# Optimization experiments

Measured on AMD Instinct MI355X. Metric: run time of the kernel, lower is better.

The kernel has to match this reference:

```python
import jax, jax.numpy as jnp
import numpy as np

D = 128          # node feature dim (input_dim)
ATT_NUM = 2      # number of attention heads (att_num)
ATT_TIMES = 2    # attention refinement iterations (att_times)
K = 1            # interact_dim from att_style 'ntn_1'
DIN2 = D * ATT_NUM   # NTN input dim = 256
FMAP = 16        # feature_map_dim
B = 8            # number of graph pairs
N = 100000       # nodes per graph
EPS = 1e-12      # F.normalize eps


def _glorot(key, shape):
    fan_in, fan_out = shape[-1], shape[-2] if len(shape) > 1 else shape[-1]
    std = np.sqrt(2.0 / (fan_in + fan_out)).astype(np.float32)
    return jax.random.normal(key, shape, dtype=jnp.float32) * std


def setup_inputs() -> dict:
    key = jax.random.key(0)
    ks = jax.random.split(key, 16)
    inp = {
        "x1": jax.random.normal(ks[0], (B, N, D), dtype=jnp.float32),
        "x2": jax.random.normal(ks[1], (B, N, D), dtype=jnp.float32),
        # Attention params (stacked over att_num heads)
        "W_att": _glorot(ks[2], (ATT_NUM, D, D)),
        "V_att": _glorot(ks[3], (ATT_NUM, K, 2 * D)),
        "Wt_att": _glorot(ks[4], (ATT_NUM, K, D, D)),
        "U_att": _glorot(ks[5], (ATT_NUM, K, 1)),
        "b_att": jax.random.normal(ks[6], (ATT_NUM, K), dtype=jnp.float32) * 0.1,
        # NTN params
        "V_ntn": _glorot(ks[7], (FMAP, 2 * DIN2)),
        "W_ntn": _glorot(ks[8], (FMAP, DIN2, DIN2)),
        "b_ntn": jax.random.normal(ks[9], (FMAP,), dtype=jnp.float32),
        # projection MLP: 16 -> 8 -> 4 -> 2 -> 1 (Linear, no bias; weight shape (out, in))
        "proj0": _glorot(ks[10], (8, 16)),
        "proj1": _glorot(ks[11], (4, 8)),
        "proj2": _glorot(ks[12], (2, 4)),
        "proj3": _glorot(ks[13], (1, 2)),
    }
    return inp


def _l1_normalize(s, axis):
    return s / jnp.maximum(jnp.sum(jnp.abs(s), axis=axis, keepdims=True), EPS)


def _attention(x, W_att, V_att, Wt_att, U_att, b_att):
    # x: (N, D)  ->  pooled graph embedding (D * ATT_NUM,)
    outs = []
    for i in range(ATT_NUM):
        xc = x
        out = None
        Va, Vb = V_att[i, :, :D], V_att[i, :, D:]   # (K, D) each
        for _ in range(ATT_TIMES):
            h = jnp.tanh(jnp.mean(xc, axis=0) @ W_att[i])        # (D,)
            # NTN-style attention scores, vectorized over all nodes
            s = xc @ Va.T + (Vb @ h)[None, :]                    # (N, K)
            s = s + jnp.einsum('nd,kde,e->nk', xc, Wt_att[i], h)
            s = s + b_att[i][None, :]
            s = _l1_normalize(s, axis=1)
            att = jax.nn.sigmoid(s) @ U_att[i]                   # (N, 1)
            out = att[:, 0] @ xc                                 # (D,)
            xc = xc * att
        outs.append(out)
    return jnp.concatenate(outs)   # (DIN2,)


def _ntn(g1, g2, V_ntn, W_ntn, b_ntn):
    # g1, g2: (DIN2,) -> (FMAP,)
    Va, Vb = V_ntn[:, :DIN2], V_ntn[:, DIN2:]
    s = Va @ g1 + Vb @ g2 + jnp.einsum('fde,d,e->f', W_ntn, g1, g2) + b_ntn
    s = s / jnp.maximum(jnp.sum(jnp.abs(s)), EPS)   # L1 normalize over the single row
    return jax.nn.relu(s)


def reference(x1, x2, W_att, V_att, Wt_att, U_att, b_att,
              V_ntn, W_ntn, b_ntn, proj0, proj1, proj2, proj3):
    def pair_fn(xa, xb):
        g1 = _attention(xa, W_att, V_att, Wt_att, U_att, b_att)
        g2 = _attention(xb, W_att, V_att, Wt_att, U_att, b_att)
        y = _ntn(g1, g2, V_ntn, W_ntn, b_ntn)      # (FMAP,)
        for Wp in (proj0, proj1, proj2, proj3):
            y = Wp @ y
        return y                                    # (1,)
    return jax.vmap(pair_fn)(x1, x2)                # (B, 1) pairwise similarity scores
```

## Files before the change

kernel.cpp:

```cpp
#include <hip/hip_runtime.h>
#include <hip/hip_bf16.h>
#include <math.h>

#define NROWS 100000
#define DIM 128
#define NGRAPH 16
#define NCHUNK 128
#define CHROWS 782
#define EPSV 1e-12f

#define SZ_SUMP (NGRAPH*NCHUNK*DIM)
#define SZ_WV   (NGRAPH*2*DIM)
#define SZ_OP   (NGRAPH*NCHUNK*2*DIM)
#define OFF_SUMP 0
#define OFF_WV1 (OFF_SUMP + SZ_SUMP)
#define OFF_C1  (OFF_WV1 + SZ_WV)
#define OFF_O1P (OFF_C1 + 32)
#define OFF_WV2 (OFF_O1P + SZ_OP)
#define OFF_C2  (OFF_WV2 + SZ_WV)
#define OFF_O2P (OFF_C2 + 32)
#define OFF_G   (OFF_O2P + SZ_OP)
#define OFF_S   (OFF_G + NGRAPH*256)

__device__ __forceinline__ const float* graph_ptr(const float* x1, const float* x2, int g) {
    return (g < 8) ? (x1 + (size_t)g * NROWS * DIM) : (x2 + (size_t)(g - 8) * NROWS * DIM);
}

__device__ __forceinline__ float red16(float x) {
    int t;
    t = __builtin_amdgcn_update_dpp(0, __float_as_int(x), 0xB1, 0xF, 0xF, true);
    x += __int_as_float(t);
    t = __builtin_amdgcn_update_dpp(0, __float_as_int(x), 0x4E, 0xF, 0xF, true);
    x += __int_as_float(t);
    t = __builtin_amdgcn_update_dpp(0, __float_as_int(x), 0x141, 0xF, 0xF, true);
    x += __int_as_float(t);
    t = __builtin_amdgcn_update_dpp(0, __float_as_int(x), 0x140, 0xF, 0xF, true);
    x += __int_as_float(t);
    return x;
}

__device__ __forceinline__ float dot8(float4 v0, float4 v1, float4 w0, float4 w1) {
    float d = v0.x * w0.x;
    d = fmaf(v0.y, w0.y, d); d = fmaf(v0.z, w0.z, d); d = fmaf(v0.w, w0.w, d);
    d = fmaf(v1.x, w1.x, d); d = fmaf(v1.y, w1.y, d); d = fmaf(v1.z, w1.z, d);
    d = fmaf(v1.w, w1.w, d);
    return d;
}

__device__ __forceinline__ float4 ld4(const float* p) {
    return *reinterpret_cast<const float4*>(p);
}

__global__ __launch_bounds__(256) void k_sum(const float* __restrict__ x1,
                                             const float* __restrict__ x2,
                                             float* __restrict__ sump) {
    int g = blockIdx.x >> 7, c = blockIdx.x & (NCHUNK - 1);
    const float* xg = graph_ptr(x1, x2, g);
    int lane = threadIdx.x & 31, grp = threadIdx.x >> 5;
    int col = lane * 4;
    float ax = 0.f, ay = 0.f, az = 0.f, aw = 0.f;
    int r0 = c * CHROWS, r1 = min(r0 + CHROWS, NROWS);
    for (int r = r0 + grp; r < r1; r += 8) {
        float4 v = ld4(xg + (size_t)r * DIM + col);
        ax += v.x; ay += v.y; az += v.z; aw += v.w;
    }
    __shared__ float4 lds[256];
    lds[threadIdx.x] = make_float4(ax, ay, az, aw);
    __syncthreads();
    if (threadIdx.x < 32) {
        float4 t = lds[threadIdx.x];
        for (int k = 1; k < 8; ++k) {
            float4 o = lds[k * 32 + threadIdx.x];
            t.x += o.x; t.y += o.y; t.z += o.z; t.w += o.w;
        }
        *reinterpret_cast<float4*>(sump + ((size_t)g * NCHUNK + c) * DIM + threadIdx.x * 4) = t;
    }
}

__global__ __launch_bounds__(128) void k_prep(const float* __restrict__ src, int phase,
                                              const float* __restrict__ W_att,
                                              const float* __restrict__ V_att,
                                              const float* __restrict__ Wt_att,
                                              const float* __restrict__ b_att,
                                              float* __restrict__ wv, float* __restrict__ cc) {
    int g = blockIdx.x >> 1, i = blockIdx.x & 1;
    int t = threadIdx.x;
    __shared__ float mean[DIM], h[DIM], red[DIM];
    float s = 0.f;
    if (phase == 1) {
        for (int c = 0; c < NCHUNK; ++c) s += src[((size_t)g * NCHUNK + c) * DIM + t];
    } else {
        for (int c = 0; c < NCHUNK; ++c) s += src[(((size_t)g * NCHUNK + c) * 2 + i) * DIM + t];
    }
    mean[t] = s / (float)NROWS;
    __syncthreads();
    const float* W = W_att + (size_t)i * DIM * DIM;
    float hv = 0.f;
    for (int d = 0; d < DIM; ++d) hv = fmaf(mean[d], W[d * DIM + t], hv);
    h[t] = tanhf(hv);
    __syncthreads();
    const float* Va = V_att + (size_t)i * 2 * DIM;
    const float* Vb = Va + DIM;
    const float* Wt = Wt_att + (size_t)i * DIM * DIM;
    float w = Va[t];
    for (int e = 0; e < DIM; ++e) w = fmaf(Wt[t * DIM + e], h[e], w);
    wv[((size_t)g * 2 + i) * DIM + t] = w;
    red[t] = Vb[t] * h[t];
    __syncthreads();
    for (int k = 64; k; k >>= 1) { if (t < k) red[t] += red[t + k]; __syncthreads(); }
    if (t == 0) cc[g * 2 + i] = red[0] + b_att[i];
}

__global__ __launch_bounds__(256) void k_pass2(const float* __restrict__ x1,
                                               const float* __restrict__ x2,
                                               const float* __restrict__ wv1,
                                               const float* __restrict__ c1,
                                               const float* __restrict__ U_att,
                                               float* __restrict__ o1p) {
    int g = blockIdx.x >> 7, c = blockIdx.x & (NCHUNK - 1);
    const float* xg = graph_ptr(x1, x2, g);
    int tid = threadIdx.x;
    int l16 = tid & 15, slot = tid >> 4;
    int colb = l16 * 8;
    float4 w0a = ld4(wv1 + ((size_t)g * 2 + 0) * DIM + colb);
    float4 w0b = ld4(wv1 + ((size_t)g * 2 + 0) * DIM + colb + 4);
    float4 w1a = ld4(wv1 + ((size_t)g * 2 + 1) * DIM + colb);
    float4 w1b = ld4(wv1 + ((size_t)g * 2 + 1) * DIM + colb + 4);
    float cc0 = c1[g * 2 + 0], cc1 = c1[g * 2 + 1];
    float u0 = U_att[0], u1 = U_att[1];
    float sp = 1.f / (1.f + expf(-1.f)), sn = 1.f / (1.f + expf(1.f));
    float ap0 = u0 * sp, an0 = u0 * sn, ap1 = u1 * sp, an1 = u1 * sn;
    float4 a0l = make_float4(0, 0, 0, 0), a0h = make_float4(0, 0, 0, 0);
    float4 a1l = make_float4(0, 0, 0, 0), a1h = make_float4(0, 0, 0, 0);
    int r0 = c * CHROWS, r1 = min(r0 + CHROWS, NROWS);
    for (int r = r0 + slot; r < r1; r += 16) {
        const float* p = xg + (size_t)r * DIM + colb;
        float4 v0 = ld4(p), v1 = ld4(p + 4);
        float d0 = red16(dot8(v0, v1, w0a, w0b));
        float d1 = red16(dot8(v0, v1, w1a, w1b));
        float at0 = (d0 + cc0 >= 0.f) ? ap0 : an0;
        float at1 = (d1 + cc1 >= 0.f) ? ap1 : an1;
        a0l.x = fmaf(at0, v0.x, a0l.x); a0l.y = fmaf(at0, v0.y, a0l.y);
        a0l.z = fmaf(at0, v0.z, a0l.z); a0l.w = fmaf(at0, v0.w, a0l.w);
        a0h.x = fmaf(at0, v1.x, a0h.x); a0h.y = fmaf(at0, v1.y, a0h.y);
        a0h.z = fmaf(at0, v1.z, a0h.z); a0h.w = fmaf(at0, v1.w, a0h.w);
        a1l.x = fmaf(at1, v0.x, a1l.x); a1l.y = fmaf(at1, v0.y, a1l.y);
        a1l.z = fmaf(at1, v0.z, a1l.z); a1l.w = fmaf(at1, v0.w, a1l.w);
        a1h.x = fmaf(at1, v1.x, a1h.x); a1h.y = fmaf(at1, v1.y, a1h.y);
        a1h.z = fmaf(at1, v1.z, a1h.z); a1h.w = fmaf(at1, v1.w, a1h.w);
    }
    __shared__ float red[2][16][DIM];
    *reinterpret_cast<float4*>(&red[0][slot][colb]) = a0l;
    *reinterpret_cast<float4*>(&red[0][slot][colb + 4]) = a0h;
    *reinterpret_cast<float4*>(&red[1][slot][colb]) = a1l;
    *reinterpret_cast<float4*>(&red[1][slot][colb + 4]) = a1h;
    __syncthreads();
    int i = tid >> 7, d = tid & 127;
    float s = 0.f;
    #pragma unroll
    for (int k = 0; k < 16; ++k) s += red[i][k][d];
    o1p[(((size_t)g * NCHUNK + c) * 2 + i) * DIM + d] = s;
}

__global__ __launch_bounds__(256) void k_pass3(const float* __restrict__ x1,
                                               const float* __restrict__ x2,
                                               const float* __restrict__ wv1,
                                               const float* __restrict__ c1,
                                               const float* __restrict__ wv2,
                                               const float* __restrict__ c2,
                                               const float* __restrict__ U_att,
                                               float* __restrict__ o2p) {
    int g = blockIdx.x >> 7, c = blockIdx.x & (NCHUNK - 1);
    const float* xg = graph_ptr(x1, x2, g);
    int tid = threadIdx.x;
    int l16 = tid & 15, slot = tid >> 4;
    int colb = l16 * 8;
    float4 wA0a = ld4(wv1 + ((size_t)g * 2 + 0) * DIM + colb);
    float4 wA0b = ld4(wv1 + ((size_t)g * 2 + 0) * DIM + colb + 4);
    float4 wA1a = ld4(wv1 + ((size_t)g * 2 + 1) * DIM + colb);
    float4 wA1b = ld4(wv1 + ((size_t)g * 2 + 1) * DIM + colb + 4);
    float4 wB0a = ld4(wv2 + ((size_t)g * 2 + 0) * DIM + colb);
    float4 wB0b = ld4(wv2 + ((size_t)g * 2 + 0) * DIM + colb + 4);
    float4 wB1a = ld4(wv2 + ((size_t)g * 2 + 1) * DIM + colb);
    float4 wB1b = ld4(wv2 + ((size_t)g * 2 + 1) * DIM + colb + 4);
    float cA0 = c1[g * 2 + 0], cA1 = c1[g * 2 + 1];
    float cB0 = c2[g * 2 + 0], cB1 = c2[g * 2 + 1];
    float u0 = U_att[0], u1 = U_att[1];
    float sp = 1.f / (1.f + expf(-1.f)), sn = 1.f / (1.f + expf(1.f));
    float ap0 = u0 * sp, an0 = u0 * sn, ap1 = u1 * sp, an1 = u1 * sn;
    float4 a0l = make_float4(0, 0, 0, 0), a0h = make_float4(0, 0, 0, 0);
    float4 a1l = make_float4(0, 0, 0, 0), a1h = make_float4(0, 0, 0, 0);
    int r0 = c * CHROWS, r1 = min(r0 + CHROWS, NROWS);
    for (int r = r0 + slot; r < r1; r += 16) {
        const float* p = xg + (size_t)r * DIM + colb;
        float4 v0 = ld4(p), v1 = ld4(p + 4);
        float dA0 = red16(dot8(v0, v1, wA0a, wA0b));
        float dA1 = red16(dot8(v0, v1, wA1a, wA1b));
        float dB0 = red16(dot8(v0, v1, wB0a, wB0b));
        float dB1 = red16(dot8(v0, v1, wB1a, wB1b));
        float at10 = (dA0 + cA0 >= 0.f) ? ap0 : an0;
        float at11 = (dA1 + cA1 >= 0.f) ? ap1 : an1;
        float at20 = (fmaf(at10, dB0, cB0) >= 0.f) ? ap0 : an0;
        float at21 = (fmaf(at11, dB1, cB1) >= 0.f) ? ap1 : an1;
        float f0 = at10 * at20, f1 = at11 * at21;
        a0l.x = fmaf(f0, v0.x, a0l.x); a0l.y = fmaf(f0, v0.y, a0l.y);
        a0l.z = fmaf(f0, v0.z, a0l.z); a0l.w = fmaf(f0, v0.w, a0l.w);
        a0h.x = fmaf(f0, v1.x, a0h.x); a0h.y = fmaf(f0, v1.y, a0h.y);
        a0h.z = fmaf(f0, v1.z, a0h.z); a0h.w = fmaf(f0, v1.w, a0h.w);
        a1l.x = fmaf(f1, v0.x, a1l.x); a1l.y = fmaf(f1, v0.y, a1l.y);
        a1l.z = fmaf(f1, v0.z, a1l.z); a1l.w = fmaf(f1, v0.w, a1l.w);
        a1h.x = fmaf(f1, v1.x, a1h.x); a1h.y = fmaf(f1, v1.y, a1h.y);
        a1h.z = fmaf(f1, v1.z, a1h.z); a1h.w = fmaf(f1, v1.w, a1h.w);
    }
    __shared__ float red[2][16][DIM];
    *reinterpret_cast<float4*>(&red[0][slot][colb]) = a0l;
    *reinterpret_cast<float4*>(&red[0][slot][colb + 4]) = a0h;
    *reinterpret_cast<float4*>(&red[1][slot][colb]) = a1l;
    *reinterpret_cast<float4*>(&red[1][slot][colb + 4]) = a1h;
    __syncthreads();
    int i = tid >> 7, d = tid & 127;
    float s = 0.f;
    #pragma unroll
    for (int k = 0; k < 16; ++k) s += red[i][k][d];
    o2p[(((size_t)g * NCHUNK + c) * 2 + i) * DIM + d] = s;
}

__global__ __launch_bounds__(256) void k_reduceG(const float* __restrict__ o2p,
                                                 float* __restrict__ gv) {
    int g = blockIdx.x, t = threadIdx.x;
    int i = t >> 7, d = t & 127;
    float s = 0.f;
    for (int c = 0; c < NCHUNK; ++c) s += o2p[(((size_t)g * NCHUNK + c) * 2 + i) * DIM + d];
    gv[(size_t)g * 256 + t] = s;
}

__global__ __launch_bounds__(256) void k_ntn(const float* __restrict__ gv,
                                             const float* __restrict__ V_ntn,
                                             const float* __restrict__ W_ntn,
                                             const float* __restrict__ b_ntn,
                                             float* __restrict__ sout) {
    int b = blockIdx.x >> 4, f = blockIdx.x & 15;
    int e = threadIdx.x;
    __shared__ float g1s[256], g2s[256], red[256];
    g1s[e] = gv[(size_t)b * 256 + e];
    g2s[e] = gv[(size_t)(8 + b) * 256 + e];
    __syncthreads();
    const float* Wf = W_ntn + (size_t)f * 256 * 256;
    float acc = 0.f;
    for (int d = 0; d < 256; ++d) acc = fmaf(Wf[(size_t)d * 256 + e], g1s[d], acc);
    float p = acc * g2s[e];
    p = fmaf(V_ntn[(size_t)f * 512 + e], g1s[e], p);
    p = fmaf(V_ntn[(size_t)f * 512 + 256 + e], g2s[e], p);
    red[e] = p;
    __syncthreads();
    for (int k = 128; k; k >>= 1) { if (e < k) red[e] += red[e + k]; __syncthreads(); }
    if (e == 0) sout[b * 16 + f] = red[0] + b_ntn[f];
}

__global__ __launch_bounds__(64) void k_out(const float* __restrict__ sout,
                                            const float* __restrict__ p0,
                                            const float* __restrict__ p1,
                                            const float* __restrict__ p2,
                                            const float* __restrict__ p3,
                                            float* __restrict__ out) {
    int b = blockIdx.x;
    if (threadIdx.x != 0) return;
    float s[16]; float l1 = 0.f;
    for (int f = 0; f < 16; ++f) { s[f] = sout[b * 16 + f]; l1 += fabsf(s[f]); }
    float inv = 1.f / fmaxf(l1, EPSV);
    float y[16];
    for (int f = 0; f < 16; ++f) { float t = s[f] * inv; y[f] = t > 0.f ? t : 0.f; }
    float v2[4], v1[8], P[16];
    for (int j = 0; j < 4; ++j) v2[j] = p3[0] * p2[j] + p3[1] * p2[4 + j];
    for (int j = 0; j < 8; ++j) { float a = 0.f; for (int k = 0; k < 4; ++k) a = fmaf(v2[k], p1[k * 8 + j], a); v1[j] = a; }
    for (int j = 0; j < 16; ++j) { float a = 0.f; for (int k = 0; k < 8; ++k) a = fmaf(v1[k], p0[k * 16 + j], a); P[j] = a; }
    float o = 0.f;
    for (int f = 0; f < 16; ++f) o = fmaf(P[f], y[f], o);
    out[b] = o;
}

extern "C" void kernel_launch(void* const* d_in, const int* in_sizes, int n_in,
                              void* d_out, int out_size, void* d_ws, size_t ws_size,
                              hipStream_t stream) {
    const float* x1    = (const float*)d_in[0];
    const float* x2    = (const float*)d_in[1];
    const float* W_att = (const float*)d_in[2];
    const float* V_att = (const float*)d_in[3];
    const float* Wt_att= (const float*)d_in[4];
    const float* U_att = (const float*)d_in[5];
    const float* b_att = (const float*)d_in[6];
    const float* V_ntn = (const float*)d_in[7];
    const float* W_ntn = (const float*)d_in[8];
    const float* b_ntn = (const float*)d_in[9];
    const float* p0    = (const float*)d_in[10];
    const float* p1    = (const float*)d_in[11];
    const float* p2    = (const float*)d_in[12];
    const float* p3    = (const float*)d_in[13];
    float* ws  = (float*)d_ws;
    float* out = (float*)d_out;

    k_sum<<<NGRAPH * NCHUNK, 256, 0, stream>>>(x1, x2, ws + OFF_SUMP);
    k_prep<<<NGRAPH * 2, 128, 0, stream>>>(ws + OFF_SUMP, 1, W_att, V_att, Wt_att, b_att,
                                           ws + OFF_WV1, ws + OFF_C1);
    k_pass2<<<NGRAPH * NCHUNK, 256, 0, stream>>>(x1, x2, ws + OFF_WV1, ws + OFF_C1, U_att,
                                                 ws + OFF_O1P);
    k_prep<<<NGRAPH * 2, 128, 0, stream>>>(ws + OFF_O1P, 2, W_att, V_att, Wt_att, b_att,
                                           ws + OFF_WV2, ws + OFF_C2);
    k_pass3<<<NGRAPH * NCHUNK, 256, 0, stream>>>(x1, x2, ws + OFF_WV1, ws + OFF_C1,
                                                 ws + OFF_WV2, ws + OFF_C2, U_att,
                                                 ws + OFF_O2P);
    k_reduceG<<<NGRAPH, 256, 0, stream>>>(ws + OFF_O2P, ws + OFF_G);
    k_ntn<<<8 * 16, 256, 0, stream>>>(ws + OFF_G, V_ntn, W_ntn, b_ntn, ws + OFF_S);
    k_out<<<8, 64, 0, stream>>>(ws + OFF_S, p0, p1, p2, p3, out);
}
```

Measured before the change: 476.2 us.

## Use nontemporal loads, parallelize prep, fuse graph reduction into NTN kernel

Streaming reads of x1/x2 in the sum and both attention passes now use nontemporal loads, and the sum loop is unrolled by two to keep more loads in flight. The prep kernel doubles to 256 threads, splits its reductions and matvecs across two halves, and stages Wt in LDS to avoid strided global reads. The separate graph-reduction kernel is removed and its chunk sum is folded into the NTN kernel, saving a launch. In exchange, each NTN block redundantly re-reduces the partial sums, and the nontemporal hint may change cache behaviour for data that is read three times.

Measured after the change: 480.4 us. About the same (+0.9%).

```diff
diff --git a/kernel.cpp b/kernel.cpp
--- a/kernel.cpp
+++ b/kernel.cpp
@@ -19,11 +19,21 @@
 #define OFF_WV2 (OFF_O1P + SZ_OP)
 #define OFF_C2  (OFF_WV2 + SZ_WV)
 #define OFF_O2P (OFF_C2 + 32)
-#define OFF_G   (OFF_O2P + SZ_OP)
-#define OFF_S   (OFF_G + NGRAPH*256)
+#define OFF_S   (OFF_O2P + SZ_OP)
+
+typedef float v4f __attribute__((ext_vector_type(4)));
 
 __device__ __forceinline__ const float* graph_ptr(const float* x1, const float* x2, int g) {
     return (g < 8) ? (x1 + (size_t)g * NROWS * DIM) : (x2 + (size_t)(g - 8) * NROWS * DIM);
+}
+
+__device__ __forceinline__ float4 ldnt4(const float* p) {
+    v4f v = __builtin_nontemporal_load(reinterpret_cast<const v4f*>(p));
+    return make_float4(v.x, v.y, v.z, v.w);
+}
+
+__device__ __forceinline__ float4 ld4(const float* p) {
+    return *reinterpret_cast<const float4*>(p);
 }
 
 __device__ __forceinline__ float red16(float x) {
@@ -47,10 +57,6 @@
     return d;
 }
 
-__device__ __forceinline__ float4 ld4(const float* p) {
-    return *reinterpret_cast<const float4*>(p);
-}
-
 __global__ __launch_bounds__(256) void k_sum(const float* __restrict__ x1,
                                              const float* __restrict__ x2,
                                              float* __restrict__ sump) {
@@ -60,9 +66,16 @@
     int col = lane * 4;
     float ax = 0.f, ay = 0.f, az = 0.f, aw = 0.f;
     int r0 = c * CHROWS, r1 = min(r0 + CHROWS, NROWS);
-    for (int r = r0 + grp; r < r1; r += 8) {
-        float4 v = ld4(xg + (size_t)r * DIM + col);
-        ax += v.x; ay += v.y; az += v.z; aw += v.w;
+    int r = r0 + grp;
+    for (; r + 8 < r1; r += 16) {
+        float4 a = ldnt4(xg + (size_t)r * DIM + col);
+        float4 b = ldnt4(xg + (size_t)(r + 8) * DIM + col);
+        ax += a.x; ay += a.y; az += a.z; aw += a.w;
+        ax += b.x; ay += b.y; az += b.z; aw += b.w;
+    }
+    if (r < r1) {
+        float4 a = ldnt4(xg + (size_t)r * DIM + col);
+        ax += a.x; ay += a.y; az += a.z; aw += a.w;
     }
     __shared__ float4 lds[256];
     lds[threadIdx.x] = make_float4(ax, ay, az, aw);
@@ -77,38 +90,47 @@
     }
 }
 
-__global__ __launch_bounds__(128) void k_prep(const float* __restrict__ src, int phase,
+__global__ __launch_bounds__(256) void k_prep(const float* __restrict__ src, int phase,
                                               const float* __restrict__ W_att,
                                               const float* __restrict__ V_att,
                                               const float* __restrict__ Wt_att,
                                               const float* __restrict__ b_att,
                                               float* __restrict__ wv, float* __restrict__ cc) {
     int g = blockIdx.x >> 1, i = blockIdx.x & 1;
-    int t = threadIdx.x;
-    __shared__ float mean[DIM], h[DIM], red[DIM];
+    int tid = threadIdx.x, t = tid & 127, half = tid >> 7;
+    __shared__ float mean[DIM], h[DIM], red2[256];
+    __shared__ float wt[DIM][DIM + 1];
+    const float* Wt = Wt_att + (size_t)i * DIM * DIM;
+    for (int idx = tid; idx < DIM * DIM; idx += 256)
+        wt[idx >> 7][idx & 127] = Wt[idx];
     float s = 0.f;
     if (phase == 1) {
-        for (int c = 0; c < NCHUNK; ++c) s += src[((size_t)g * NCHUNK + c) * DIM + t];
+        for (int c = half; c < NCHUNK; c += 2) s += src[((size_t)g * NCHUNK + c) * DIM + t];
     } else {
-        for (int c = 0; c < NCHUNK; ++c) s += src[(((size_t)g * NCHUNK + c) * 2 + i) * DIM + t];
-    }
-    mean[t] = s / (float)NROWS;
+        for (int c = half; c < NCHUNK; c += 2) s += src[(((size_t)g * NCHUNK + c) * 2 + i) * DIM + t];
+    }
+    red2[tid] = s; __syncthreads();
+    if (half == 0) mean[t] = (red2[t] + red2[t + 128]) * (1.f / (float)NROWS);
     __syncthreads();
     const float* W = W_att + (size_t)i * DIM * DIM;
     float hv = 0.f;
-    for (int d = 0; d < DIM; ++d) hv = fmaf(mean[d], W[d * DIM + t], hv);
-    h[t] = tanhf(hv);
-    __syncthreads();
+    for (int d = half * 64; d < half * 64 + 64; ++d) hv = fmaf(mean[d], W[d * DIM + t], hv);
+    red2[tid] = hv; __syncthreads();
+    if (half == 0) h[t] = tanhf(red2[t] + red2[t + 128]);
+    __syncthreads();
+    float w = 0.f;
+    for (int e = half * 64; e < half * 64 + 64; ++e) w = fmaf(wt[t][e], h[e], w);
+    red2[tid] = w; __syncthreads();
     const float* Va = V_att + (size_t)i * 2 * DIM;
-    const float* Vb = Va + DIM;
-    const float* Wt = Wt_att + (size_t)i * DIM * DIM;
-    float w = Va[t];
-    for (int e = 0; e < DIM; ++e) w = fmaf(Wt[t * DIM + e], h[e], w);
-    wv[((size_t)g * 2 + i) * DIM + t] = w;
-    red[t] = Vb[t] * h[t];
-    __syncthreads();
-    for (int k = 64; k; k >>= 1) { if (t < k) red[t] += red[t + k]; __syncthreads(); }
-    if (t == 0) cc[g * 2 + i] = red[0] + b_att[i];
+    if (half == 0) wv[((size_t)g * 2 + i) * DIM + t] = Va[t] + red2[t] + red2[t + 128];
+    __syncthreads();
+    if (half == 0) red2[t] = Va[DIM + t] * h[t];
+    __syncthreads();
+    for (int k = 64; k; k >>= 1) {
+        if (tid < k) red2[tid] += red2[tid + k];
+        __syncthreads();
+    }
+    if (tid == 0) cc[g * 2 + i] = red2[0] + b_att[i];
 }
 
 __global__ __launch_bounds__(256) void k_pass2(const float* __restrict__ x1,
@@ -135,7 +157,7 @@
     int r0 = c * CHROWS, r1 = min(r0 + CHROWS, NROWS);
     for (int r = r0 + slot; r < r1; r += 16) {
         const float* p = xg + (size_t)r * DIM + colb;
-        float4 v0 = ld4(p), v1 = ld4(p + 4);
+        float4 v0 = ldnt4(p), v1 = ldnt4(p + 4);
         float d0 = red16(dot8(v0, v1, w0a, w0b));
         float d1 = red16(dot8(v0, v1, w1a, w1b));
         float at0 = (d0 + cc0 >= 0.f) ? ap0 : an0;
@@ -193,7 +215,7 @@
     int r0 = c * CHROWS, r1 = min(r0 + CHROWS, NROWS);
     for (int r = r0 + slot; r < r1; r += 16) {
         const float* p = xg + (size_t)r * DIM + colb;
-        float4 v0 = ld4(p), v1 = ld4(p + 4);
+        float4 v0 = ldnt4(p), v1 = ldnt4(p + 4);
         float dA0 = red16(dot8(v0, v1, wA0a, wA0b));
         float dA1 = red16(dot8(v0, v1, wA1a, wA1b));
         float dB0 = red16(dot8(v0, v1, wB0a, wB0b));
@@ -225,16 +247,7 @@
     o2p[(((size_t)g * NCHUNK + c) * 2 + i) * DIM + d] = s;
 }
 
-__global__ __launch_bounds__(256) void k_reduceG(const float* __restrict__ o2p,
-                                                 float* __restrict__ gv) {
-    int g = blockIdx.x, t = threadIdx.x;
-    int i = t >> 7, d = t & 127;
-    float s = 0.f;
-    for (int c = 0; c < NCHUNK; ++c) s += o2p[(((size_t)g * NCHUNK + c) * 2 + i) * DIM + d];
-    gv[(size_t)g * 256 + t] = s;
-}
-
-__global__ __launch_bounds__(256) void k_ntn(const float* __restrict__ gv,
+__global__ __launch_bounds__(256) void k_ntn(const float* __restrict__ o2p,
                                              const float* __restrict__ V_ntn,
                                              const float* __restrict__ W_ntn,
                                              const float* __restrict__ b_ntn,
@@ -242,18 +255,26 @@
     int b = blockIdx.x >> 4, f = blockIdx.x & 15;
     int e = threadIdx.x;
     __shared__ float g1s[256], g2s[256], red[256];
-    g1s[e] = gv[(size_t)b * 256 + e];
-    g2s[e] = gv[(size_t)(8 + b) * 256 + e];
+    int i = e >> 7, d = e & 127;
+    float s1 = 0.f, s2 = 0.f;
+    for (int c = 0; c < NCHUNK; ++c) {
+        s1 += o2p[(((size_t)b * NCHUNK + c) * 2 + i) * DIM + d];
+        s2 += o2p[(((size_t)(8 + b) * NCHUNK + c) * 2 + i) * DIM + d];
+    }
+    g1s[e] = s1; g2s[e] = s2;
     __syncthreads();
     const float* Wf = W_ntn + (size_t)f * 256 * 256;
     float acc = 0.f;
-    for (int d = 0; d < 256; ++d) acc = fmaf(Wf[(size_t)d * 256 + e], g1s[d], acc);
+    for (int dd = 0; dd < 256; ++dd) acc = fmaf(Wf[(size_t)dd * 256 + e], g1s[dd], acc);
     float p = acc * g2s[e];
     p = fmaf(V_ntn[(size_t)f * 512 + e], g1s[e], p);
     p = fmaf(V_ntn[(size_t)f * 512 + 256 + e], g2s[e], p);
     red[e] = p;
     __syncthreads();
-    for (int k = 128; k; k >>= 1) { if (e < k) red[e] += red[e + k]; __syncthreads(); }
+    for (int k = 128; k; k >>= 1) {
+        if (e < k) red[e] += red[e + k];
+        __syncthreads();
+    }
     if (e == 0) sout[b * 16 + f] = red[0] + b_ntn[f];
 }
 
@@ -300,16 +321,15 @@
     float* out = (float*)d_out;
 
     k_sum<<<NGRAPH * NCHUNK, 256, 0, stream>>>(x1, x2, ws + OFF_SUMP);
-    k_prep<<<NGRAPH * 2, 128, 0, stream>>>(ws + OFF_SUMP, 1, W_att, V_att, Wt_att, b_att,
+    k_prep<<<NGRAPH * 2, 256, 0, stream>>>(ws + OFF_SUMP, 1, W_att, V_att, Wt_att, b_att,
                                            ws + OFF_WV1, ws + OFF_C1);
     k_pass2<<<NGRAPH * NCHUNK, 256, 0, stream>>>(x1, x2, ws + OFF_WV1, ws + OFF_C1, U_att,
                                                  ws + OFF_O1P);
-    k_prep<<<NGRAPH * 2, 128, 0, stream>>>(ws + OFF_O1P, 2, W_att, V_att, Wt_att, b_att,
+    k_prep<<<NGRAPH * 2, 256, 0, stream>>>(ws + OFF_O1P, 2, W_att, V_att, Wt_att, b_att,
                                            ws + OFF_WV2, ws + OFF_C2);
     k_pass3<<<NGRAPH * NCHUNK, 256, 0, stream>>>(x1, x2, ws + OFF_WV1, ws + OFF_C1,
                                                  ws + OFF_WV2, ws + OFF_C2, U_att,
                                                  ws + OFF_O2P);
-    k_reduceG<<<NGRAPH, 256, 0, stream>>>(ws + OFF_O2P, ws + OFF_G);
-    k_ntn<<<8 * 16, 256, 0, stream>>>(ws + OFF_G, V_ntn, W_ntn, b_ntn, ws + OFF_S);
+    k_ntn<<<8 * 16, 256, 0, stream>>>(ws + OFF_O2P, V_ntn, W_ntn, b_ntn, ws + OFF_S);
     k_out<<<8, 64, 0, stream>>>(ws + OFF_S, p0, p1, p2, p3, out);
 }
```
